# Kernel tuning notes

Measured on AMD Instinct MI355X. Metric: run time of the kernel, lower is better.

Reference implementation:

```python
import jax, jax.numpy as jnp
import numpy as np

# TT configuration (matches init_kwargs)
IN_SHAPE = [8, 8, 8, 8]
OUT_SHAPE = [8, 8, 8, 8]
RANKS = [1, 3, 3, 3, 1]
BATCH = 8192


def _tt_meta():
    """Replicates cores_shape / cores_indexes construction (then reversed, as in __init__)."""
    shapes, idxs = [], []
    off = 0
    for k in range(len(IN_SHAPE)):
        # matrix view used in forward: (n_k * r_{k+1}, r_k * m_k)
        shapes.append((IN_SHAPE[k] * RANKS[k + 1], RANKS[k] * OUT_SHAPE[k]))
        size = RANKS[k] * IN_SHAPE[k] * OUT_SHAPE[k] * RANKS[k + 1]
        idxs.append((off, off + size))
        off += size
    return shapes[::-1], idxs[::-1], off


def setup_inputs() -> dict:
    shapes, idxs, total = _tt_meta()
    key = jax.random.key(0)
    k1, k2 = jax.random.split(key)
    x = jax.random.normal(k1, (BATCH, int(np.prod(IN_SHAPE))), dtype=jnp.float32)
    # orthogonal-QR init in the original only affects values; scale ~0.1/glorot is tiny
    glorot = (np.prod(IN_SHAPE) * np.prod(RANKS)) ** (1.0 / len(IN_SHAPE))
    cores_arr = jax.random.normal(k2, (total,), dtype=jnp.float32) * jnp.float32(0.1 / glorot)
    bias = jnp.zeros((int(np.prod(OUT_SHAPE)),), dtype=jnp.float32)
    return {"x": x, "cores_arr": cores_arr, "bias": bias}


def reference(x, cores_arr, bias):
    shapes, idxs, _ = _tt_meta()
    B = x.shape[0]
    for i, (shape, (a, b)) in enumerate(zip(shapes, idxs)):
        # flat core slice reinterpreted as (n_k*r_{k+1}, r_k*m_k) -- pure reshape, no transpose,
        # exactly matching torch's .view(shape) on the contiguous flat parameter.
        core = jax.lax.dynamic_slice(cores_arr, (a,), (b - a,)).reshape(shape)
        x = x.reshape(B, -1, shape[0])          # (B, rest, n_k*r_{k+1})
        x = jnp.einsum('bij,jk->bik', x, core)  # (B, rest, r_k*m_k)
        x = x.reshape(B, -1, OUT_SHAPE[-1 - i]) # fold m_k to the tail
    return x.reshape(B, -1) + bias
```

## Files before the change

kernel.cpp:

```cpp
#include <hip/hip_runtime.h>


typedef float f32x4 __attribute__((ext_vector_type(4)));

#define TOTAL_THREADS 524288
#define NBLOCKS       4194304
#define ITERS         8

__global__ void __launch_bounds__(256) tt_fused(const float* __restrict__ x,
                                                const float* __restrict__ cores,
                                                const float* __restrict__ bias,
                                                float* __restrict__ out) {
    __shared__ float c[1536];
    __shared__ float T1[192];
    __shared__ float T2[192];
    __shared__ __align__(16) float Ms[64];
    const int t = threadIdx.x;
    for (int i = t; i < 1536; i += 256) c[i] = cores[i];
    __syncthreads();
    const float* A0 = c + 1344;
    const float* A1 = c + 768;
    const float* A2 = c + 192;
    const float* A3 = c + 0;
    if (t < 192) {
        int r = t / 24, k = t % 24;
        float s = 0.f;
        #pragma unroll
        for (int j = 0; j < 24; ++j) s = fmaf(A0[r * 24 + j], A1[j * 24 + k], s);
        T1[t] = s;
    }
    __syncthreads();
    if (t < 192) {
        int r = t / 24, k = t % 24;
        float s = 0.f;
        #pragma unroll
        for (int j = 0; j < 24; ++j) s = fmaf(T1[r * 24 + j], A2[j * 24 + k], s);
        T2[t] = s;
    }
    __syncthreads();
    if (t < 64) {
        int r = t / 8, m = t % 8;
        float s = 0.f;
        #pragma unroll
        for (int j = 0; j < 24; ++j) s = fmaf(T2[r * 24 + j], A3[j * 8 + m], s);
        Ms[t] = s;
    }
    __syncthreads();

    f32x4 Mr[16];
    #pragma unroll
    for (int i = 0; i < 16; ++i) Mr[i] = *reinterpret_cast<const f32x4*>(&Ms[i * 4]);

    const int tid = blockIdx.x * 256 + threadIdx.x;

    const int col = (tid & 511) * 8;
    const f32x4 bb0 = *reinterpret_cast<const f32x4*>(bias + col);
    const f32x4 bb1 = *reinterpret_cast<const f32x4*>(bias + col + 4);

    #pragma unroll 4
    for (int k = 0; k < ITERS; ++k) {
        const size_t p = (size_t)tid + (size_t)k * TOTAL_THREADS;
        const f32x4* xp = reinterpret_cast<const f32x4*>(x + p * 8);
        const f32x4 a = xp[0];
        const f32x4 b = xp[1];

        f32x4 acc0 = bb0;
        f32x4 acc1 = bb1;
        const float xv[8] = {a.x, a.y, a.z, a.w, b.x, b.y, b.z, b.w};
        #pragma unroll
        for (int j = 0; j < 8; ++j) {
            acc0 += xv[j] * Mr[2 * j];
            acc1 += xv[j] * Mr[2 * j + 1];
        }

        f32x4* op = reinterpret_cast<f32x4*>(out + p * 8);
        __builtin_nontemporal_store(acc0, op);
        __builtin_nontemporal_store(acc1, op + 1);
    }
}

extern "C" void kernel_launch(void* const* d_in, const int* in_sizes, int n_in,
                              void* d_out, int out_size, void* d_ws, size_t ws_size,
                              hipStream_t stream) {
    const float* x     = (const float*)d_in[0];
    const float* cores = (const float*)d_in[1];
    const float* bias  = (const float*)d_in[2];
    float* out = (float*)d_out;

    tt_fused<<<2048, 256, 0, stream>>>(x, cores, bias, out);
}
```

Measured before the change: 52.12 us.

## Split each 8-wide row across two lanes with shuffle reduction

Each thread now loads and stores one 16-byte vector instead of two, with pairs of adjacent lanes splitting each 8-element row. Each lane computes partial products for both output halves using half of the 8x8 matrix, then the lanes exchange partial sums through cross-lane xor shuffles. This makes consecutive lanes touch consecutive 16-byte chunks, for better coalesced global access, and halves the per-thread matrix register footprint. In exchange it adds four shuffles per iteration and doubles the iteration count. It also replaces the nontemporal stores with regular stores.

```diff
diff --git a/kernel.cpp b/kernel.cpp
--- a/kernel.cpp
+++ b/kernel.cpp
@@ -4,8 +4,8 @@
 typedef float f32x4 __attribute__((ext_vector_type(4)));
 
 #define TOTAL_THREADS 524288
-#define NBLOCKS       4194304
-#define ITERS         8
+#define NHALF         8388608
+#define ITERS         16
 
 __global__ void __launch_bounds__(256) tt_fused(const float* __restrict__ x,
                                                 const float* __restrict__ cores,
@@ -47,35 +47,35 @@
     }
     __syncthreads();
 
-    f32x4 Mr[16];
-    #pragma unroll
-    for (int i = 0; i < 16; ++i) Mr[i] = *reinterpret_cast<const f32x4*>(&Ms[i * 4]);
+    const int gid = blockIdx.x * 256 + threadIdx.x;
+    const int h = gid & 1;
 
-    const int tid = blockIdx.x * 256 + threadIdx.x;
+    f32x4 Msel[8];
+    {
+        const f32x4* Mb = reinterpret_cast<const f32x4*>(&Ms[h * 32]);
+        #pragma unroll
+        for (int i = 0; i < 8; ++i) Msel[i] = Mb[i];
+    }
 
-    const int col = (tid & 511) * 8;
-    const f32x4 bb0 = *reinterpret_cast<const f32x4*>(bias + col);
-    const f32x4 bb1 = *reinterpret_cast<const f32x4*>(bias + col + 4);
+    const f32x4 bb = *reinterpret_cast<const f32x4*>(bias + 4 * (gid & 1023));
 
     #pragma unroll 4
     for (int k = 0; k < ITERS; ++k) {
-        const size_t p = (size_t)tid + (size_t)k * TOTAL_THREADS;
-        const f32x4* xp = reinterpret_cast<const f32x4*>(x + p * 8);
-        const f32x4 a = xp[0];
-        const f32x4 b = xp[1];
+        const size_t g = (size_t)gid + (size_t)k * TOTAL_THREADS;
+        const f32x4 v = *reinterpret_cast<const f32x4*>(x + g * 4);
 
-        f32x4 acc0 = bb0;
-        f32x4 acc1 = bb1;
-        const float xv[8] = {a.x, a.y, a.z, a.w, b.x, b.y, b.z, b.w};
-        #pragma unroll
-        for (int j = 0; j < 8; ++j) {
-            acc0 += xv[j] * Mr[2 * j];
-            acc1 += xv[j] * Mr[2 * j + 1];
-        }
+        f32x4 P0 = v.x * Msel[0] + v.y * Msel[2] + v.z * Msel[4] + v.w * Msel[6];
+        f32x4 P1 = v.x * Msel[1] + v.y * Msel[3] + v.z * Msel[5] + v.w * Msel[7];
 
-        f32x4* op = reinterpret_cast<f32x4*>(out + p * 8);
-        __builtin_nontemporal_store(acc0, op);
-        __builtin_nontemporal_store(acc1, op + 1);
+        f32x4 S = h ? P0 : P1;
+        f32x4 R;
+        R.x = __shfl_xor(S.x, 1);
+        R.y = __shfl_xor(S.y, 1);
+        R.z = __shfl_xor(S.z, 1);
+        R.w = __shfl_xor(S.w, 1);
+
+        const f32x4 res = (h ? P1 : P0) + R + bb;
+        *reinterpret_cast<f32x4*>(out + g * 4) = res;
     }
 }
 
```

Result: faster. 49.32 us (-5.4%).
